# Performance work log

Measured on AMD Instinct MI355X. Metric: run time of the kernel, lower is better.

## Reference

```python
import jax, jax.numpy as jnp
import numpy as np

N_NODES = 100000
N_REL = 8
F_IN, F_HID, F_OUT = 64, 64, 32
N_EDGES = 1000000


def rgcn_conv(x, W, root, bias, src, dst, edge_type):
    """PyG RGCNConv with default aggr='mean': out[i] = sum_r mean_{j in N_r(i)} W_r x_j + root x_i + bias."""
    R, _, O = W.shape
    N = x.shape[0]
    # Transform every node under every relation: [R, N, O]
    h = jnp.einsum('nf,rfo->rno', x, W)
    # Gather per-edge messages: [E, O]
    msg = h[edge_type, src]
    # Per-(relation, dst) mean aggregation via combined segment ids
    seg = edge_type * N + dst
    sums = jax.ops.segment_sum(msg, seg, num_segments=R * N).reshape(R, N, O)
    cnt = jax.ops.segment_sum(jnp.ones((msg.shape[0],), msg.dtype), seg,
                              num_segments=R * N).reshape(R, N, 1)
    mean = sums / jnp.maximum(cnt, 1.0)  # empty neighborhoods -> 0
    return mean.sum(axis=0) + x @ root + bias


def setup_inputs() -> dict:
    key = jax.random.key(0)
    ks = jax.random.split(key, 9)
    s = lambda fan: 1.0 / np.sqrt(fan)
    x = jax.random.normal(ks[0], (N_NODES, F_IN), jnp.float32)
    edge_index = jax.random.randint(ks[1], (2, N_EDGES), 0, N_NODES, jnp.int64)
    edge_type = jax.random.randint(ks[2], (N_EDGES,), 0, N_REL, jnp.int64)
    W1 = jax.random.normal(ks[3], (N_REL, F_IN, F_HID), jnp.float32) * s(F_IN)
    root1 = jax.random.normal(ks[4], (F_IN, F_HID), jnp.float32) * s(F_IN)
    b1 = jnp.zeros((F_HID,), jnp.float32)
    W2 = jax.random.normal(ks[5], (N_REL, F_HID, F_OUT), jnp.float32) * s(F_HID)
    root2 = jax.random.normal(ks[6], (F_HID, F_OUT), jnp.float32) * s(F_HID)
    b2 = jnp.zeros((F_OUT,), jnp.float32)
    return {"x": x, "W1": W1, "root1": root1, "b1": b1,
            "W2": W2, "root2": root2, "b2": b2,
            "edge_index": edge_index, "edge_type": edge_type}


def reference(x, W1, root1, b1, W2, root2, b2, edge_index, edge_type):
    src, dst = edge_index[0], edge_index[1]
    # encode (dropout is identity in eval mode)
    h = jax.nn.relu(rgcn_conv(x, W1, root1, b1, src, dst, edge_type))
    z = rgcn_conv(h, W2, root2, b2, src, dst, edge_type)
    # decode: gather-dot-product link scores over the same edge list
    return (z[src] * z[dst]).sum(axis=1)
```

## Files before the change

kernel.cpp:

```cpp
#include <hip/hip_runtime.h>

#define F_IN 64
#define F_HID 64
#define F_OUT 32
#define NREL 8
#define SCAP 6144
#define RCAP 10240
#define MAXBUCK 200
#define PA_PE 16

typedef __attribute__((ext_vector_type(8))) short bfrag;
typedef __attribute__((ext_vector_type(4))) float ffrag;

__device__ inline unsigned short f2bf(float f) {
  unsigned u = __float_as_uint(f);
  unsigned r = (u + 0x7fffu + ((u >> 16) & 1u)) >> 16;
  return (unsigned short)r;
}
__device__ inline unsigned bf16pair(float lo, float hi) {
  return (unsigned)f2bf(lo) | ((unsigned)f2bf(hi) << 16);
}
__device__ inline float bflo(unsigned u) { return __uint_as_float(u << 16); }
__device__ inline float bfhi(unsigned u) { return __uint_as_float(u & 0xffff0000u); }

__device__ inline void acc8(float (&acc)[8], float s, uint4 g) {
  acc[0] += s * bflo(g.x); acc[1] += s * bfhi(g.x);
  acc[2] += s * bflo(g.y); acc[3] += s * bfhi(g.y);
  acc[4] += s * bflo(g.z); acc[5] += s * bfhi(g.z);
  acc[6] += s * bflo(g.w); acc[7] += s * bfhi(g.w);
}
__device__ inline float dot8(uint4 a, uint4 b) {
  return bflo(a.x) * bflo(b.x) + bfhi(a.x) * bfhi(b.x) +
         bflo(a.y) * bflo(b.y) + bfhi(a.y) * bfhi(b.y) +
         bflo(a.z) * bflo(b.z) + bfhi(a.z) * bfhi(b.z) +
         bflo(a.w) * bflo(b.w) + bfhi(a.w) * bfhi(b.w);
}

template <int O, bool PERMK>
__device__ inline void wprep_one(int t, const float* __restrict__ W,
                                 const float* __restrict__ root,
                                 unsigned short* __restrict__ Wf) {
  constexpr int CT = O / 16;
  int l = t & 63;
  int s = (t >> 6) & 1;
  int rc = t >> 7;
  int c = rc % CT;
  int r = rc / CT;
  const float* wsrc = (r < NREL) ? W + (size_t)r * 64 * O : root;
  unsigned short* dst = Wf + (size_t)t * 8;
  int col = c * 16 + (l & 15);
  int k0 = s * 32 + ((l >> 4) * 8);
#pragma unroll
  for (int j = 0; j < 8; ++j) {
    int k = k0 + j;
    if (PERMK) k = (k & 3) * 16 + (k >> 2);
    dst[j] = f2bf(wsrc[(size_t)k * O + col]);
  }
}

__global__ __launch_bounds__(256) void prep_kernel(
    const float* __restrict__ W1, const float* __restrict__ root1,
    const float* __restrict__ W2, const float* __restrict__ root2,
    unsigned short* __restrict__ wf1, unsigned short* __restrict__ wf2,
    int* __restrict__ gcur, int nbuck) {
  int gid = blockIdx.x * 256 + threadIdx.x;
  const int J1 = (NREL + 1) * (F_HID / 16) * 2 * 64;
  const int J2 = (NREL + 1) * (F_OUT / 16) * 2 * 64;
  if (gid < J1) {
    wprep_one<F_HID, false>(gid, W1, root1, wf1);
  } else if (gid < J1 + J2) {
    wprep_one<F_OUT, true>(gid - J1, W2, root2, wf2);
  } else if (gid - J1 - J2 < nbuck) {
    int b = gid - J1 - J2;
    gcur[b] = b * SCAP;
  }
}

__global__ __launch_bounds__(256) void binA_kernel(
    const int* __restrict__ src, const int* __restrict__ dst,
    const int* __restrict__ et, int* __restrict__ gcur,
    unsigned* __restrict__ staging, int E) {
  __shared__ int hist[MAXBUCK * 4];
  __shared__ int wbase[MAXBUCK * 4];
  const int tid = threadIdx.x;
  const int wave = tid >> 6;
  for (int i = tid; i < MAXBUCK * 4; i += 256) hist[i] = 0;
  __syncthreads();
  const int base = blockIdx.x * (256 * PA_PE);
  int dv[PA_PE], rk[PA_PE];
#pragma unroll
  for (int j = 0; j < PA_PE; ++j) {
    int e = base + j * 256 + tid;
    if (e < E) {
      int d = dst[e];
      dv[j] = d;
      rk[j] = atomicAdd(&hist[(d >> 9) * 4 + wave], 1);
    } else {
      dv[j] = -1;
    }
  }
  __syncthreads();
  for (int b = tid; b < MAXBUCK; b += 256) {
    int h0 = hist[b * 4 + 0], h1 = hist[b * 4 + 1];
    int h2 = hist[b * 4 + 2], h3 = hist[b * 4 + 3];
    int tot = h0 + h1 + h2 + h3;
    int gb = tot ? atomicAdd(&gcur[b], tot) : 0;
    wbase[b * 4 + 0] = gb;
    wbase[b * 4 + 1] = gb + h0;
    wbase[b * 4 + 2] = gb + h0 + h1;
    wbase[b * 4 + 3] = gb + h0 + h1 + h2;
  }
  __syncthreads();
#pragma unroll
  for (int j = 0; j < PA_PE; ++j) {
    if (dv[j] >= 0) {
      int e = base + j * 256 + tid;
      unsigned pk = (unsigned)src[e] | ((unsigned)et[e] << 17) |
                    ((unsigned)(dv[j] & 511) << 20);
      staging[wbase[(dv[j] >> 9) * 4 + wave] + rk[j]] = pk;
    }
  }
}

__device__ void binB_body(
    int b, const unsigned* __restrict__ staging, const int* __restrict__ gcur,
    int2* __restrict__ rec, int* __restrict__ startsA, int* __restrict__ endsA,
    int N) {
  __shared__ int cnt8[512 * 8];
  __shared__ int cur[512];
  __shared__ int tsum[256];
  const int tid = threadIdx.x;
  const int n0 = b << 9;
  const int nn = min(512, N - n0);
  const int cnt_b = gcur[b] - b * SCAP;
  const unsigned* st = staging + (size_t)b * SCAP;
  for (int i = tid; i < 512 * 8; i += 256) cnt8[i] = 0;
  __syncthreads();
  for (int i = tid; i < cnt_b; i += 256) {
    unsigned e = st[i];
    atomicAdd(&cnt8[((e >> 20) & 511) * 8 + ((e >> 17) & 7)], 1);
  }
  __syncthreads();
  const int na = 2 * tid, nb = 2 * tid + 1;
  int deg0 = 0, deg1 = 0;
#pragma unroll
  for (int r = 0; r < 8; ++r) {
    deg0 += cnt8[na * 8 + r];
    deg1 += cnt8[nb * 8 + r];
  }
  const int pd0 = (deg0 + 7) & ~7, pd1 = (deg1 + 7) & ~7;
  tsum[tid] = pd0 + pd1;
  __syncthreads();
  for (int off = 1; off < 256; off <<= 1) {
    int v = (tid >= off) ? tsum[tid - off] : 0;
    __syncthreads();
    tsum[tid] += v;
    __syncthreads();
  }
  const int excl = tsum[tid] - (pd0 + pd1);
  const int s0 = b * RCAP + excl;
  const int s1 = s0 + pd0;
  if (na < nn) { startsA[n0 + na] = s0; endsA[n0 + na] = s0 + pd0; cur[na] = s0; }
  if (nb < nn) { startsA[n0 + nb] = s1; endsA[n0 + nb] = s1 + pd1; cur[nb] = s1; }
  __syncthreads();
  for (int i = tid; i < 512 * 8; i += 256) {
    int cc = cnt8[i];
    ((float*)cnt8)[i] = cc > 0 ? 1.0f / (float)cc : 0.0f;
  }
  __syncthreads();
  for (int i = tid; i < cnt_b; i += 256) {
    unsigned e = st[i];
    int s = e & 0x1FFFF;
    int r = (e >> 17) & 7;
    int dl = (e >> 20) & 511;
    int pos = atomicAdd(&cur[dl], 1);
    rec[pos] = make_int2(r * N + s, ((const int*)cnt8)[dl * 8 + r]);
  }
  __syncthreads();
  if (na < nn) for (int p = cur[na]; p < s0 + pd0; ++p) rec[p] = make_int2(0, 0);
  if (nb < nn) for (int p = cur[nb]; p < s1 + pd1; ++p) rec[p] = make_int2(0, 0);
}

template <int O, bool F32IN>
__device__ void transform_body(int blk, const void* __restrict__ Xv,
                               const unsigned short* __restrict__ Wf,
                               unsigned short* __restrict__ H, int N) {
  constexpr int CT = O / 16;
  const int w = threadIdx.x >> 6;
  const int l = threadIdx.x & 63;
  const int nb = blk * 64;
  int arow = nb + w * 16 + (l & 15);
  if (arow >= N) arow = N - 1;
  bfrag a0, a1;
  if (F32IN) {
    const float* xf = (const float*)Xv + (size_t)arow * 64 + ((l >> 4) * 8);
    float4 v0 = *(const float4*)(xf);
    float4 v1 = *(const float4*)(xf + 4);
    float4 v2 = *(const float4*)(xf + 32);
    float4 v3 = *(const float4*)(xf + 36);
    a0[0] = (short)f2bf(v0.x); a0[1] = (short)f2bf(v0.y);
    a0[2] = (short)f2bf(v0.z); a0[3] = (short)f2bf(v0.w);
    a0[4] = (short)f2bf(v1.x); a0[5] = (short)f2bf(v1.y);
    a0[6] = (short)f2bf(v1.z); a0[7] = (short)f2bf(v1.w);
    a1[0] = (short)f2bf(v2.x); a1[1] = (short)f2bf(v2.y);
    a1[2] = (short)f2bf(v2.z); a1[3] = (short)f2bf(v2.w);
    a1[4] = (short)f2bf(v3.x); a1[5] = (short)f2bf(v3.y);
    a1[6] = (short)f2bf(v3.z); a1[7] = (short)f2bf(v3.w);
  } else {
    const unsigned short* xp = (const unsigned short*)Xv + (size_t)arow * 64 + ((l >> 4) * 8);
    a0 = *(const bfrag*)(xp);
    a1 = *(const bfrag*)(xp + 32);
  }
  const int rbase = nb + w * 16 + ((l >> 4) << 2);
  for (int r = 0; r < NREL + 1; ++r) {
    const unsigned short* wb = Wf + ((size_t)r * CT * 2 * 64 + l) * 8;
    ffrag acc[CT];
#pragma unroll
    for (int c = 0; c < CT; ++c) {
      bfrag b0 = *(const bfrag*)(wb + (size_t)(c * 2 + 0) * 512);
      bfrag b1 = *(const bfrag*)(wb + (size_t)(c * 2 + 1) * 512);
      ffrag z = {0.f, 0.f, 0.f, 0.f};
      acc[c] = __builtin_amdgcn_mfma_f32_16x16x32_bf16(a0, b0, z, 0, 0, 0);
      acc[c] = __builtin_amdgcn_mfma_f32_16x16x32_bf16(a1, b1, acc[c], 0, 0, 0);
    }
#pragma unroll
    for (int i = 0; i < 4; ++i) {
      int row = rbase + i;
      if (row < N) {
        if (O == 64) {
          uint2 v;
          v.x = bf16pair(acc[0][i], acc[1][i]);
          v.y = bf16pair(acc[2][i], acc[3][i]);
          *(uint2*)(H + ((size_t)r * N + row) * 64 + (l & 15) * 4) = v;
        } else {
          *(unsigned*)(H + ((size_t)r * N + row) * 32 + (l & 15) * 2) =
              bf16pair(acc[0][i], acc[1][i]);
        }
      }
    }
  }
}

__global__ __launch_bounds__(256) void binB_t1_kernel(
    const unsigned* __restrict__ staging, const int* __restrict__ gcur,
    int2* __restrict__ rec, int* __restrict__ startsA, int* __restrict__ endsA,
    int nbuck, const float* __restrict__ x,
    const unsigned short* __restrict__ wf1, unsigned short* __restrict__ h,
    int N) {
  if ((int)blockIdx.x < nbuck) {
    binB_body((int)blockIdx.x, staging, gcur, rec, startsA, endsA, N);
  } else {
    transform_body<F_HID, true>((int)blockIdx.x - nbuck, x, wf1, h, N);
  }
}

__global__ __launch_bounds__(256) void transform2_kernel(
    const unsigned short* __restrict__ Xb, const unsigned short* __restrict__ Wf,
    unsigned short* __restrict__ H, int N) {
  transform_body<F_OUT, false>((int)blockIdx.x, Xb, Wf, H, N);
}

template <int O, bool RELU>
__global__ __launch_bounds__(256) void csr_agg_kernel(
    const unsigned* __restrict__ H, const int* __restrict__ startsA,
    const int* __restrict__ endsA, const int2* __restrict__ rec,
    const float* __restrict__ bias, unsigned* __restrict__ Y, int N) {
  constexpr int C = O / 8;
  constexpr int NPB = 256 / C;
  constexpr int HROW = O / 2;
  constexpr int CT = O / 16;
  int t = threadIdx.x;
  int n = blockIdx.x * NPB + t / C;
  int c = t % C;
  if (n >= N) return;
  float acc[8];
  uint4 rr = *(const uint4*)(H + ((size_t)(NREL * N) + n) * HROW + c * 4);
#pragma unroll
  for (int j = 0; j < 8; ++j) {
    int q = c * 8 + j;
    acc[j] = bias[(q % CT) * 16 + q / CT];
  }
  acc[0] += bflo(rr.x); acc[1] += bfhi(rr.x);
  acc[2] += bflo(rr.y); acc[3] += bfhi(rr.y);
  acc[4] += bflo(rr.z); acc[5] += bfhi(rr.z);
  acc[6] += bflo(rr.w); acc[7] += bfhi(rr.w);
  int p = startsA[n];
  int end = endsA[n];
  for (; p < end; p += 8) {
    int4 e01 = *(const int4*)(rec + p);
    int4 e23 = *(const int4*)(rec + p + 2);
    int4 e45 = *(const int4*)(rec + p + 4);
    int4 e67 = *(const int4*)(rec + p + 6);
    uint4 g0 = *(const uint4*)(H + (size_t)e01.x * HROW + c * 4);
    uint4 g1 = *(const uint4*)(H + (size_t)e01.z * HROW + c * 4);
    uint4 g2 = *(const uint4*)(H + (size_t)e23.x * HROW + c * 4);
    uint4 g3 = *(const uint4*)(H + (size_t)e23.z * HROW + c * 4);
    uint4 g4 = *(const uint4*)(H + (size_t)e45.x * HROW + c * 4);
    uint4 g5 = *(const uint4*)(H + (size_t)e45.z * HROW + c * 4);
    uint4 g6 = *(const uint4*)(H + (size_t)e67.x * HROW + c * 4);
    uint4 g7 = *(const uint4*)(H + (size_t)e67.z * HROW + c * 4);
    acc8(acc, __int_as_float(e01.y), g0);
    acc8(acc, __int_as_float(e01.w), g1);
    acc8(acc, __int_as_float(e23.y), g2);
    acc8(acc, __int_as_float(e23.w), g3);
    acc8(acc, __int_as_float(e45.y), g4);
    acc8(acc, __int_as_float(e45.w), g5);
    acc8(acc, __int_as_float(e67.y), g6);
    acc8(acc, __int_as_float(e67.w), g7);
  }
  if (RELU) {
#pragma unroll
    for (int j = 0; j < 8; ++j) acc[j] = fmaxf(acc[j], 0.f);
  }
  uint4 o;
  o.x = bf16pair(acc[0], acc[1]);
  o.y = bf16pair(acc[2], acc[3]);
  o.z = bf16pair(acc[4], acc[5]);
  o.w = bf16pair(acc[6], acc[7]);
  *(uint4*)(Y + (size_t)n * HROW + c * 4) = o;
}

__global__ __launch_bounds__(256) void decode_kernel(
    const unsigned* __restrict__ Z, const int* __restrict__ src,
    const int* __restrict__ dst, float* __restrict__ out, int E) {
  int e = blockIdx.x * blockDim.x + threadIdx.x;
  if (e >= E) return;
  const uint4* zs = (const uint4*)(Z + (size_t)src[e] * 16);
  const uint4* zd = (const uint4*)(Z + (size_t)dst[e] * 16);
  uint4 a0 = zs[0], a1 = zs[1], a2 = zs[2], a3 = zs[3];
  uint4 b0 = zd[0], b1 = zd[1], b2 = zd[2], b3 = zd[3];
  out[e] = dot8(a0, b0) + dot8(a1, b1) + dot8(a2, b2) + dot8(a3, b3);
}

extern "C" void kernel_launch(void* const* d_in, const int* in_sizes, int n_in,
                              void* d_out, int out_size, void* d_ws, size_t ws_size,
                              hipStream_t stream) {
  const float* x     = (const float*)d_in[0];
  const float* W1    = (const float*)d_in[1];
  const float* root1 = (const float*)d_in[2];
  const float* b1    = (const float*)d_in[3];
  const float* W2    = (const float*)d_in[4];
  const float* root2 = (const float*)d_in[5];
  const float* b2    = (const float*)d_in[6];
  const int*   ei    = (const int*)d_in[7];
  const int*   et    = (const int*)d_in[8];

  const int N = in_sizes[0] / F_IN;
  const int E = in_sizes[8];
  const int nbuck = (N + 511) >> 9;
  const int nbinA = (E + 256 * PA_PE - 1) / (256 * PA_PE);
  const int nT1 = (N + 63) / 64;
  const int* srcp = ei;
  const int* dstp = ei + E;

  char* ws = (char*)d_ws;
  int*            gcur    = (int*)(ws + 0);
  unsigned*       staging = (unsigned*)(ws + 4096);
  int*            startsA = (int*)(ws + 4919296);
  int*            endsA   = (int*)(ws + 5319296);
  int2*           rec     = (int2*)(ws + 5719296);
  unsigned short* wf1     = (unsigned short*)(ws + 21775616);
  unsigned short* wf2     = (unsigned short*)(ws + 21849344);
  unsigned short* h       = (unsigned short*)(ws + 21886208);
  unsigned short* hmid    = (unsigned short*)(ws + 137086208);
  unsigned short* z       = (unsigned short*)(ws + 149886208);

  prep_kernel<<<28, 256, 0, stream>>>(W1, root1, W2, root2, wf1, wf2, gcur, nbuck);

  binA_kernel<<<nbinA, 256, 0, stream>>>(srcp, dstp, et, gcur, staging, E);

  binB_t1_kernel<<<nbuck + nT1, 256, 0, stream>>>(
      staging, gcur, rec, startsA, endsA, nbuck, x, wf1, h, N);

  csr_agg_kernel<F_HID, true>
      <<<(N + 31) / 32, 256, 0, stream>>>((const unsigned*)h, startsA, endsA, rec,
                                          b1, (unsigned*)hmid, N);

  transform2_kernel<<<(N + 63) / 64, 256, 0, stream>>>(hmid, wf2, h, N);
  csr_agg_kernel<F_OUT, false>
      <<<(N + 63) / 64, 256, 0, stream>>>((const unsigned*)h, startsA, endsA, rec,
                                          b2, (unsigned*)z, N);

  decode_kernel<<<(E + 255) / 256, 256, 0, stream>>>((const unsigned*)z, srcp, dstp,
                                                     (float*)d_out, E);
}
```

Before: 155.6 us.

## Move root-weight transform from MFMA transform into aggregation kernels as fp32 FMAs

The root (self-loop) projection is no longer computed as a ninth relation in the MFMA transform kernels and stored to H. Each aggregation thread now reads the node's input row and multiplies it by a pre-permuted fp32 root matrix in registers. This removes one of nine transform outputs per layer, cutting the H writes and the later reads, at the cost of extra scalar FMA work and root-matrix loads in the aggregation kernel. Root weights are now applied in fp32 rather than bf16, which slightly changes numerics.

```diff
diff --git a/kernel.cpp b/kernel.cpp
--- a/kernel.cpp
+++ b/kernel.cpp
@@ -36,9 +36,26 @@
          bflo(a.w) * bflo(b.w) + bfhi(a.w) * bfhi(b.w);
 }
 
+__device__ inline void fma8_rows(float (&acc)[8], float4 xv,
+                                 const float* __restrict__ r0,
+                                 const float* __restrict__ r1,
+                                 const float* __restrict__ r2,
+                                 const float* __restrict__ r3) {
+#pragma unroll
+  for (int h = 0; h < 2; ++h) {
+    float4 a0 = *(const float4*)(r0 + h * 4);
+    float4 a1 = *(const float4*)(r1 + h * 4);
+    float4 a2 = *(const float4*)(r2 + h * 4);
+    float4 a3 = *(const float4*)(r3 + h * 4);
+    acc[h * 4 + 0] += xv.x * a0.x + xv.y * a1.x + xv.z * a2.x + xv.w * a3.x;
+    acc[h * 4 + 1] += xv.x * a0.y + xv.y * a1.y + xv.z * a2.y + xv.w * a3.y;
+    acc[h * 4 + 2] += xv.x * a0.z + xv.y * a1.z + xv.z * a2.z + xv.w * a3.z;
+    acc[h * 4 + 3] += xv.x * a0.w + xv.y * a1.w + xv.z * a2.w + xv.w * a3.w;
+  }
+}
+
 template <int O, bool PERMK>
 __device__ inline void wprep_one(int t, const float* __restrict__ W,
-                                 const float* __restrict__ root,
                                  unsigned short* __restrict__ Wf) {
   constexpr int CT = O / 16;
   int l = t & 63;
@@ -46,7 +63,7 @@
   int rc = t >> 7;
   int c = rc % CT;
   int r = rc / CT;
-  const float* wsrc = (r < NREL) ? W + (size_t)r * 64 * O : root;
+  const float* wsrc = W + (size_t)r * 64 * O;
   unsigned short* dst = Wf + (size_t)t * 8;
   int col = c * 16 + (l & 15);
   int k0 = s * 32 + ((l >> 4) * 8);
@@ -62,16 +79,26 @@
     const float* __restrict__ W1, const float* __restrict__ root1,
     const float* __restrict__ W2, const float* __restrict__ root2,
     unsigned short* __restrict__ wf1, unsigned short* __restrict__ wf2,
+    float* __restrict__ rootp1, float* __restrict__ rootp2,
     int* __restrict__ gcur, int nbuck) {
   int gid = blockIdx.x * 256 + threadIdx.x;
-  const int J1 = (NREL + 1) * (F_HID / 16) * 2 * 64;
-  const int J2 = (NREL + 1) * (F_OUT / 16) * 2 * 64;
+  const int J1 = NREL * (F_HID / 16) * 2 * 64;
+  const int J2 = NREL * (F_OUT / 16) * 2 * 64;
   if (gid < J1) {
-    wprep_one<F_HID, false>(gid, W1, root1, wf1);
+    wprep_one<F_HID, false>(gid, W1, wf1);
   } else if (gid < J1 + J2) {
-    wprep_one<F_OUT, true>(gid - J1, W2, root2, wf2);
-  } else if (gid - J1 - J2 < nbuck) {
-    int b = gid - J1 - J2;
+    wprep_one<F_OUT, true>(gid - J1, W2, wf2);
+  } else if (gid < J1 + J2 + 4096) {
+    int i = gid - J1 - J2;
+    int q = i & 63, k = i >> 6;
+    rootp1[i] = root1[(size_t)k * 64 + ((q & 3) * 16 + (q >> 2))];
+  } else if (gid < J1 + J2 + 4096 + 2048) {
+    int i = gid - J1 - J2 - 4096;
+    int q = i & 31, s = i >> 5;
+    rootp2[i] = root2[(size_t)((s & 3) * 16 + (s >> 2)) * 32 +
+                      ((q & 1) * 16 + (q >> 1))];
+  } else if (gid - J1 - J2 - 4096 - 2048 < nbuck) {
+    int b = gid - J1 - J2 - 4096 - 2048;
     gcur[b] = b * SCAP;
   }
 }
@@ -212,7 +239,7 @@
     a1 = *(const bfrag*)(xp + 32);
   }
   const int rbase = nb + w * 16 + ((l >> 4) << 2);
-  for (int r = 0; r < NREL + 1; ++r) {
+  for (int r = 0; r < NREL; ++r) {
     const unsigned short* wb = Wf + ((size_t)r * CT * 2 * 64 + l) * 8;
     ffrag acc[CT];
 #pragma unroll
@@ -260,10 +287,11 @@
   transform_body<F_OUT, false>((int)blockIdx.x, Xb, Wf, H, N);
 }
 
-template <int O, bool RELU>
+template <int O, bool RELU, bool XBF>
 __global__ __launch_bounds__(256) void csr_agg_kernel(
     const unsigned* __restrict__ H, const int* __restrict__ startsA,
     const int* __restrict__ endsA, const int2* __restrict__ rec,
+    const void* __restrict__ Xin, const float* __restrict__ rootp,
     const float* __restrict__ bias, unsigned* __restrict__ Y, int N) {
   constexpr int C = O / 8;
   constexpr int NPB = 256 / C;
@@ -274,16 +302,33 @@
   int c = t % C;
   if (n >= N) return;
   float acc[8];
-  uint4 rr = *(const uint4*)(H + ((size_t)(NREL * N) + n) * HROW + c * 4);
 #pragma unroll
   for (int j = 0; j < 8; ++j) {
     int q = c * 8 + j;
     acc[j] = bias[(q % CT) * 16 + q / CT];
   }
-  acc[0] += bflo(rr.x); acc[1] += bfhi(rr.x);
-  acc[2] += bflo(rr.y); acc[3] += bfhi(rr.y);
-  acc[4] += bflo(rr.z); acc[5] += bfhi(rr.z);
-  acc[6] += bflo(rr.w); acc[7] += bfhi(rr.w);
+  const float* Rb = rootp + c * 8;
+  if (!XBF) {
+    const float* xr = (const float*)Xin + (size_t)n * 64;
+#pragma unroll 4
+    for (int k = 0; k < 64; k += 4) {
+      float4 xv = *(const float4*)(xr + k);
+      fma8_rows(acc, xv, Rb + (size_t)(k + 0) * O, Rb + (size_t)(k + 1) * O,
+                Rb + (size_t)(k + 2) * O, Rb + (size_t)(k + 3) * O);
+    }
+  } else {
+    const unsigned* xr = (const unsigned*)Xin + (size_t)n * 32;
+#pragma unroll 2
+    for (int k = 0; k < 64; k += 8) {
+      uint4 raw = *(const uint4*)(xr + k / 2);
+      float4 x0 = make_float4(bflo(raw.x), bfhi(raw.x), bflo(raw.y), bfhi(raw.y));
+      float4 x1 = make_float4(bflo(raw.z), bfhi(raw.z), bflo(raw.w), bfhi(raw.w));
+      fma8_rows(acc, x0, Rb + (size_t)(k + 0) * O, Rb + (size_t)(k + 1) * O,
+                Rb + (size_t)(k + 2) * O, Rb + (size_t)(k + 3) * O);
+      fma8_rows(acc, x1, Rb + (size_t)(k + 4) * O, Rb + (size_t)(k + 5) * O,
+                Rb + (size_t)(k + 6) * O, Rb + (size_t)(k + 7) * O);
+    }
+  }
   int p = startsA[n];
   int end = endsA[n];
   for (; p < end; p += 8) {
@@ -360,26 +405,29 @@
   int*            endsA   = (int*)(ws + 5319296);
   int2*           rec     = (int2*)(ws + 5719296);
   unsigned short* wf1     = (unsigned short*)(ws + 21775616);
-  unsigned short* wf2     = (unsigned short*)(ws + 21849344);
-  unsigned short* h       = (unsigned short*)(ws + 21886208);
-  unsigned short* hmid    = (unsigned short*)(ws + 137086208);
-  unsigned short* z       = (unsigned short*)(ws + 149886208);
-
-  prep_kernel<<<28, 256, 0, stream>>>(W1, root1, W2, root2, wf1, wf2, gcur, nbuck);
+  unsigned short* wf2     = (unsigned short*)(ws + 21841152);
+  float*          rootp1  = (float*)(ws + 21873920);
+  float*          rootp2  = (float*)(ws + 21890304);
+  unsigned short* h       = (unsigned short*)(ws + 21898496);
+  unsigned short* hmid    = (unsigned short*)(ws + 124298496);
+  unsigned short* z       = (unsigned short*)(ws + 137098496);
+
+  prep_kernel<<<49, 256, 0, stream>>>(W1, root1, W2, root2, wf1, wf2,
+                                      rootp1, rootp2, gcur, nbuck);
 
   binA_kernel<<<nbinA, 256, 0, stream>>>(srcp, dstp, et, gcur, staging, E);
 
   binB_t1_kernel<<<nbuck + nT1, 256, 0, stream>>>(
       staging, gcur, rec, startsA, endsA, nbuck, x, wf1, h, N);
 
-  csr_agg_kernel<F_HID, true>
+  csr_agg_kernel<F_HID, true, false>
       <<<(N + 31) / 32, 256, 0, stream>>>((const unsigned*)h, startsA, endsA, rec,
-                                          b1, (unsigned*)hmid, N);
+                                          x, rootp1, b1, (unsigned*)hmid, N);
 
   transform2_kernel<<<(N + 63) / 64, 256, 0, stream>>>(hmid, wf2, h, N);
-  csr_agg_kernel<F_OUT, false>
+  csr_agg_kernel<F_OUT, false, true>
       <<<(N + 63) / 64, 256, 0, stream>>>((const unsigned*)h, startsA, endsA, rec,
-                                          b2, (unsigned*)z, N);
+                                          hmid, rootp2, b2, (unsigned*)z, N);
 
   decode_kernel<<<(E + 255) / 256, 256, 0, stream>>>((const unsigned*)z, srcp, dstp,
                                                      (float*)d_out, E);
```

New measurement: 209.8 us. +34.8%, slower.

## Fuse layer-1 aggregation with layer-2 transform via shared-memory tile

Applied to the files above, without the earlier changes.

Merges the first-layer CSR mean aggregation with the second-layer MFMA transform in one 512-thread kernel. Aggregated rows for 64 nodes are staged in LDS and fed straight into MFMA, so the hmid intermediate is never written to or read back from global memory and one launch is dropped. h2 now gets its own buffer instead of overwriting h1. The cost is a block-wide barrier between the irregular gather phase and the matmul phase, a larger block that may lower occupancy, and load imbalance from nodes with uneven degree.

```diff
diff --git a/kernel.cpp b/kernel.cpp
--- a/kernel.cpp
+++ b/kernel.cpp
@@ -181,42 +181,34 @@
   if (nb < nn) for (int p = cur[nb]; p < s1 + pd1; ++p) rec[p] = make_int2(0, 0);
 }
 
-template <int O, bool F32IN>
-__device__ void transform_body(int blk, const void* __restrict__ Xv,
-                               const unsigned short* __restrict__ Wf,
-                               unsigned short* __restrict__ H, int N) {
-  constexpr int CT = O / 16;
+__device__ void transform1_body(int blk, const float* __restrict__ Xv,
+                                const unsigned short* __restrict__ Wf,
+                                unsigned short* __restrict__ H, int N) {
   const int w = threadIdx.x >> 6;
   const int l = threadIdx.x & 63;
   const int nb = blk * 64;
   int arow = nb + w * 16 + (l & 15);
   if (arow >= N) arow = N - 1;
   bfrag a0, a1;
-  if (F32IN) {
-    const float* xf = (const float*)Xv + (size_t)arow * 64 + ((l >> 4) * 8);
-    float4 v0 = *(const float4*)(xf);
-    float4 v1 = *(const float4*)(xf + 4);
-    float4 v2 = *(const float4*)(xf + 32);
-    float4 v3 = *(const float4*)(xf + 36);
-    a0[0] = (short)f2bf(v0.x); a0[1] = (short)f2bf(v0.y);
-    a0[2] = (short)f2bf(v0.z); a0[3] = (short)f2bf(v0.w);
-    a0[4] = (short)f2bf(v1.x); a0[5] = (short)f2bf(v1.y);
-    a0[6] = (short)f2bf(v1.z); a0[7] = (short)f2bf(v1.w);
-    a1[0] = (short)f2bf(v2.x); a1[1] = (short)f2bf(v2.y);
-    a1[2] = (short)f2bf(v2.z); a1[3] = (short)f2bf(v2.w);
-    a1[4] = (short)f2bf(v3.x); a1[5] = (short)f2bf(v3.y);
-    a1[6] = (short)f2bf(v3.z); a1[7] = (short)f2bf(v3.w);
-  } else {
-    const unsigned short* xp = (const unsigned short*)Xv + (size_t)arow * 64 + ((l >> 4) * 8);
-    a0 = *(const bfrag*)(xp);
-    a1 = *(const bfrag*)(xp + 32);
-  }
+  const float* xf = Xv + (size_t)arow * 64 + ((l >> 4) * 8);
+  float4 v0 = *(const float4*)(xf);
+  float4 v1 = *(const float4*)(xf + 4);
+  float4 v2 = *(const float4*)(xf + 32);
+  float4 v3 = *(const float4*)(xf + 36);
+  a0[0] = (short)f2bf(v0.x); a0[1] = (short)f2bf(v0.y);
+  a0[2] = (short)f2bf(v0.z); a0[3] = (short)f2bf(v0.w);
+  a0[4] = (short)f2bf(v1.x); a0[5] = (short)f2bf(v1.y);
+  a0[6] = (short)f2bf(v1.z); a0[7] = (short)f2bf(v1.w);
+  a1[0] = (short)f2bf(v2.x); a1[1] = (short)f2bf(v2.y);
+  a1[2] = (short)f2bf(v2.z); a1[3] = (short)f2bf(v2.w);
+  a1[4] = (short)f2bf(v3.x); a1[5] = (short)f2bf(v3.y);
+  a1[6] = (short)f2bf(v3.z); a1[7] = (short)f2bf(v3.w);
   const int rbase = nb + w * 16 + ((l >> 4) << 2);
   for (int r = 0; r < NREL + 1; ++r) {
-    const unsigned short* wb = Wf + ((size_t)r * CT * 2 * 64 + l) * 8;
-    ffrag acc[CT];
-#pragma unroll
-    for (int c = 0; c < CT; ++c) {
+    const unsigned short* wb = Wf + ((size_t)r * 4 * 2 * 64 + l) * 8;
+    ffrag acc[4];
+#pragma unroll
+    for (int c = 0; c < 4; ++c) {
       bfrag b0 = *(const bfrag*)(wb + (size_t)(c * 2 + 0) * 512);
       bfrag b1 = *(const bfrag*)(wb + (size_t)(c * 2 + 1) * 512);
       ffrag z = {0.f, 0.f, 0.f, 0.f};
@@ -227,15 +219,10 @@
     for (int i = 0; i < 4; ++i) {
       int row = rbase + i;
       if (row < N) {
-        if (O == 64) {
-          uint2 v;
-          v.x = bf16pair(acc[0][i], acc[1][i]);
-          v.y = bf16pair(acc[2][i], acc[3][i]);
-          *(uint2*)(H + ((size_t)r * N + row) * 64 + (l & 15) * 4) = v;
-        } else {
-          *(unsigned*)(H + ((size_t)r * N + row) * 32 + (l & 15) * 2) =
-              bf16pair(acc[0][i], acc[1][i]);
-        }
+        uint2 v;
+        v.x = bf16pair(acc[0][i], acc[1][i]);
+        v.y = bf16pair(acc[2][i], acc[3][i]);
+        *(uint2*)(H + ((size_t)r * N + row) * 64 + (l & 15) * 4) = v;
       }
     }
   }
@@ -250,35 +237,117 @@
   if ((int)blockIdx.x < nbuck) {
     binB_body((int)blockIdx.x, staging, gcur, rec, startsA, endsA, N);
   } else {
-    transform_body<F_HID, true>((int)blockIdx.x - nbuck, x, wf1, h, N);
-  }
-}
-
-__global__ __launch_bounds__(256) void transform2_kernel(
-    const unsigned short* __restrict__ Xb, const unsigned short* __restrict__ Wf,
-    unsigned short* __restrict__ H, int N) {
-  transform_body<F_OUT, false>((int)blockIdx.x, Xb, Wf, H, N);
-}
-
-template <int O, bool RELU>
-__global__ __launch_bounds__(256) void csr_agg_kernel(
+    transform1_body((int)blockIdx.x - nbuck, x, wf1, h, N);
+  }
+}
+
+__global__ __launch_bounds__(512) void agg1_t2_kernel(
+    const unsigned* __restrict__ H1, const int* __restrict__ startsA,
+    const int* __restrict__ endsA, const int2* __restrict__ rec,
+    const float* __restrict__ b1, const unsigned short* __restrict__ wf2,
+    unsigned short* __restrict__ h2, int N) {
+  __shared__ unsigned short hm[64 * 72];
+  const int t = threadIdx.x;
+  const int nb = (int)blockIdx.x * 64;
+  {
+    const int loc = t >> 3;
+    const int c = t & 7;
+    const int n = nb + loc;
+    const bool valid = (n < N);
+    const int nl = valid ? n : 0;
+    float acc[8];
+#pragma unroll
+    for (int j = 0; j < 8; ++j) {
+      int q = c * 8 + j;
+      acc[j] = b1[(q & 3) * 16 + (q >> 2)];
+    }
+    uint4 rr = *(const uint4*)(H1 + ((size_t)(NREL * N) + nl) * 32 + c * 4);
+    acc[0] += bflo(rr.x); acc[1] += bfhi(rr.x);
+    acc[2] += bflo(rr.y); acc[3] += bfhi(rr.y);
+    acc[4] += bflo(rr.z); acc[5] += bfhi(rr.z);
+    acc[6] += bflo(rr.w); acc[7] += bfhi(rr.w);
+    int p = valid ? startsA[nl] : 0;
+    int end = valid ? endsA[nl] : 0;
+    for (; p < end; p += 8) {
+      int4 e01 = *(const int4*)(rec + p);
+      int4 e23 = *(const int4*)(rec + p + 2);
+      int4 e45 = *(const int4*)(rec + p + 4);
+      int4 e67 = *(const int4*)(rec + p + 6);
+      uint4 g0 = *(const uint4*)(H1 + (size_t)e01.x * 32 + c * 4);
+      uint4 g1 = *(const uint4*)(H1 + (size_t)e01.z * 32 + c * 4);
+      uint4 g2 = *(const uint4*)(H1 + (size_t)e23.x * 32 + c * 4);
+      uint4 g3 = *(const uint4*)(H1 + (size_t)e23.z * 32 + c * 4);
+      uint4 g4 = *(const uint4*)(H1 + (size_t)e45.x * 32 + c * 4);
+      uint4 g5 = *(const uint4*)(H1 + (size_t)e45.z * 32 + c * 4);
+      uint4 g6 = *(const uint4*)(H1 + (size_t)e67.x * 32 + c * 4);
+      uint4 g7 = *(const uint4*)(H1 + (size_t)e67.z * 32 + c * 4);
+      acc8(acc, __int_as_float(e01.y), g0);
+      acc8(acc, __int_as_float(e01.w), g1);
+      acc8(acc, __int_as_float(e23.y), g2);
+      acc8(acc, __int_as_float(e23.w), g3);
+      acc8(acc, __int_as_float(e45.y), g4);
+      acc8(acc, __int_as_float(e45.w), g5);
+      acc8(acc, __int_as_float(e67.y), g6);
+      acc8(acc, __int_as_float(e67.w), g7);
+    }
+#pragma unroll
+    for (int j = 0; j < 8; ++j) acc[j] = fmaxf(acc[j], 0.f);
+    uint4 o;
+    o.x = bf16pair(acc[0], acc[1]);
+    o.y = bf16pair(acc[2], acc[3]);
+    o.z = bf16pair(acc[4], acc[5]);
+    o.w = bf16pair(acc[6], acc[7]);
+    *(uint4*)&hm[loc * 72 + c * 8] = o;
+  }
+  __syncthreads();
+  {
+    const int w = t >> 6;
+    const int l = t & 63;
+    const int w4 = w & 3;
+    const int rh = w >> 2;
+    const int rloc = w4 * 16 + (l & 15);
+    bfrag a0 = *(const bfrag*)&hm[rloc * 72 + ((l >> 4) << 3)];
+    bfrag a1 = *(const bfrag*)&hm[rloc * 72 + 32 + ((l >> 4) << 3)];
+    const int rbase = nb + w4 * 16 + ((l >> 4) << 2);
+    const int r0 = rh ? 4 : 0;
+    const int r1 = rh ? 9 : 4;
+    for (int r = r0; r < r1; ++r) {
+      const unsigned short* wb = wf2 + ((size_t)r * 2 * 2 * 64 + l) * 8;
+      ffrag acc[2];
+#pragma unroll
+      for (int c = 0; c < 2; ++c) {
+        bfrag b0 = *(const bfrag*)(wb + (size_t)(c * 2 + 0) * 512);
+        bfrag b1 = *(const bfrag*)(wb + (size_t)(c * 2 + 1) * 512);
+        ffrag z = {0.f, 0.f, 0.f, 0.f};
+        acc[c] = __builtin_amdgcn_mfma_f32_16x16x32_bf16(a0, b0, z, 0, 0, 0);
+        acc[c] = __builtin_amdgcn_mfma_f32_16x16x32_bf16(a1, b1, acc[c], 0, 0, 0);
+      }
+#pragma unroll
+      for (int i = 0; i < 4; ++i) {
+        int row = rbase + i;
+        if (row < N) {
+          *(unsigned*)(h2 + ((size_t)r * N + row) * 32 + (l & 15) * 2) =
+              bf16pair(acc[0][i], acc[1][i]);
+        }
+      }
+    }
+  }
+}
+
+__global__ __launch_bounds__(256) void agg2_kernel(
     const unsigned* __restrict__ H, const int* __restrict__ startsA,
     const int* __restrict__ endsA, const int2* __restrict__ rec,
     const float* __restrict__ bias, unsigned* __restrict__ Y, int N) {
-  constexpr int C = O / 8;
-  constexpr int NPB = 256 / C;
-  constexpr int HROW = O / 2;
-  constexpr int CT = O / 16;
   int t = threadIdx.x;
-  int n = blockIdx.x * NPB + t / C;
-  int c = t % C;
+  int n = blockIdx.x * 64 + t / 4;
+  int c = t & 3;
   if (n >= N) return;
   float acc[8];
-  uint4 rr = *(const uint4*)(H + ((size_t)(NREL * N) + n) * HROW + c * 4);
+  uint4 rr = *(const uint4*)(H + ((size_t)(NREL * N) + n) * 16 + c * 4);
 #pragma unroll
   for (int j = 0; j < 8; ++j) {
     int q = c * 8 + j;
-    acc[j] = bias[(q % CT) * 16 + q / CT];
+    acc[j] = bias[(q & 1) * 16 + (q >> 1)];
   }
   acc[0] += bflo(rr.x); acc[1] += bfhi(rr.x);
   acc[2] += bflo(rr.y); acc[3] += bfhi(rr.y);
@@ -291,14 +360,14 @@
     int4 e23 = *(const int4*)(rec + p + 2);
     int4 e45 = *(const int4*)(rec + p + 4);
     int4 e67 = *(const int4*)(rec + p + 6);
-    uint4 g0 = *(const uint4*)(H + (size_t)e01.x * HROW + c * 4);
-    uint4 g1 = *(const uint4*)(H + (size_t)e01.z * HROW + c * 4);
-    uint4 g2 = *(const uint4*)(H + (size_t)e23.x * HROW + c * 4);
-    uint4 g3 = *(const uint4*)(H + (size_t)e23.z * HROW + c * 4);
-    uint4 g4 = *(const uint4*)(H + (size_t)e45.x * HROW + c * 4);
-    uint4 g5 = *(const uint4*)(H + (size_t)e45.z * HROW + c * 4);
-    uint4 g6 = *(const uint4*)(H + (size_t)e67.x * HROW + c * 4);
-    uint4 g7 = *(const uint4*)(H + (size_t)e67.z * HROW + c * 4);
+    uint4 g0 = *(const uint4*)(H + (size_t)e01.x * 16 + c * 4);
+    uint4 g1 = *(const uint4*)(H + (size_t)e01.z * 16 + c * 4);
+    uint4 g2 = *(const uint4*)(H + (size_t)e23.x * 16 + c * 4);
+    uint4 g3 = *(const uint4*)(H + (size_t)e23.z * 16 + c * 4);
+    uint4 g4 = *(const uint4*)(H + (size_t)e45.x * 16 + c * 4);
+    uint4 g5 = *(const uint4*)(H + (size_t)e45.z * 16 + c * 4);
+    uint4 g6 = *(const uint4*)(H + (size_t)e67.x * 16 + c * 4);
+    uint4 g7 = *(const uint4*)(H + (size_t)e67.z * 16 + c * 4);
     acc8(acc, __int_as_float(e01.y), g0);
     acc8(acc, __int_as_float(e01.w), g1);
     acc8(acc, __int_as_float(e23.y), g2);
@@ -308,16 +377,12 @@
     acc8(acc, __int_as_float(e67.y), g6);
     acc8(acc, __int_as_float(e67.w), g7);
   }
-  if (RELU) {
-#pragma unroll
-    for (int j = 0; j < 8; ++j) acc[j] = fmaxf(acc[j], 0.f);
-  }
   uint4 o;
   o.x = bf16pair(acc[0], acc[1]);
   o.y = bf16pair(acc[2], acc[3]);
   o.z = bf16pair(acc[4], acc[5]);
   o.w = bf16pair(acc[6], acc[7]);
-  *(uint4*)(Y + (size_t)n * HROW + c * 4) = o;
+  *(uint4*)(Y + (size_t)n * 16 + c * 4) = o;
 }
 
 __global__ __launch_bounds__(256) void decode_kernel(
@@ -350,6 +415,7 @@
   const int nbuck = (N + 511) >> 9;
   const int nbinA = (E + 256 * PA_PE - 1) / (256 * PA_PE);
   const int nT1 = (N + 63) / 64;
+  const int nB64 = (N + 63) / 64;
   const int* srcp = ei;
   const int* dstp = ei + E;
 
@@ -361,25 +427,22 @@
   int2*           rec     = (int2*)(ws + 5719296);
   unsigned short* wf1     = (unsigned short*)(ws + 21775616);
   unsigned short* wf2     = (unsigned short*)(ws + 21849344);
-  unsigned short* h       = (unsigned short*)(ws + 21886208);
-  unsigned short* hmid    = (unsigned short*)(ws + 137086208);
-  unsigned short* z       = (unsigned short*)(ws + 149886208);
+  unsigned short* h1      = (unsigned short*)(ws + 21886208);
+  unsigned short* h2      = (unsigned short*)(ws + 137086208);
+  unsigned short* z       = (unsigned short*)(ws + 194686208);
 
   prep_kernel<<<28, 256, 0, stream>>>(W1, root1, W2, root2, wf1, wf2, gcur, nbuck);
 
   binA_kernel<<<nbinA, 256, 0, stream>>>(srcp, dstp, et, gcur, staging, E);
 
   binB_t1_kernel<<<nbuck + nT1, 256, 0, stream>>>(
-      staging, gcur, rec, startsA, endsA, nbuck, x, wf1, h, N);
-
-  csr_agg_kernel<F_HID, true>
-      <<<(N + 31) / 32, 256, 0, stream>>>((const unsigned*)h, startsA, endsA, rec,
-                                          b1, (unsigned*)hmid, N);
-
-  transform2_kernel<<<(N + 63) / 64, 256, 0, stream>>>(hmid, wf2, h, N);
-  csr_agg_kernel<F_OUT, false>
-      <<<(N + 63) / 64, 256, 0, stream>>>((const unsigned*)h, startsA, endsA, rec,
-                                          b2, (unsigned*)z, N);
+      staging, gcur, rec, startsA, endsA, nbuck, x, wf1, h1, N);
+
+  agg1_t2_kernel<<<nB64, 512, 0, stream>>>(
+      (const unsigned*)h1, startsA, endsA, rec, b1, wf2, h2, N);
+
+  agg2_kernel<<<nB64, 256, 0, stream>>>(
+      (const unsigned*)h2, startsA, endsA, rec, b2, (unsigned*)z, N);
 
   decode_kernel<<<(E + 255) / 256, 256, 0, stream>>>((const unsigned*)z, srcp, dstp,
                                                      (float*)d_out, E);
```

After: 157.3 us. Within noise of the previous version (+1.0%).
